# Kernel optimization log

Hardware: AMD Instinct MI355X
Metric: run time of the kernel (lower is better)

## Reference

```python
import jax, jax.numpy as jnp
import numpy as np

B, C, H = 32, 1, 384
K = 378  # cropped size per ProbaV cPSNR spec
NSHIFT = 7  # u, v each in [0, 7)


def _crops(target):
    # 49 shifted 378x378 crops of the HR target -> [49, B, C, K, K]
    return jnp.stack([target[:, :, u:u + K, v:v + K]
                      for u in range(NSHIFT) for v in range(NSHIFT)])


def setup_inputs() -> dict:
    key = jax.random.key(0)
    k1, k2, k3 = jax.random.split(key, 3)
    # scale to [0, 255) so the HR > 5 validity mask is nontrivial
    pred = jax.random.uniform(k1, (B, C, H, H), dtype=jnp.float32) * 255.0
    target = jax.random.uniform(k2, (B, C, H, H), dtype=jnp.float32) * 255.0
    blended_target = jax.random.uniform(k3, (B, C, H, H), dtype=jnp.float32) * 255.0
    return {"pred": pred, "target": target, "blended_target": blended_target}


def reference(pred, target, blended_target):
    # SR: center crop of the super-resolved prediction
    SR = pred[:, :, 3:3 + K, 3:3 + K]                      # [B, C, K, K]
    HR = _crops(target)                                     # [49, B, C, K, K]
    mask = (HR > 5.0).astype(SR.dtype)                      # validity mask per shift
    denom = jnp.sum(mask, axis=(1, 2, 3, 4))                # [49]
    co = 1.0 / denom
    # brightness bias b per shift (masked mean of HR - SR)
    b = co * jnp.sum((HR - SR) * mask, axis=(1, 2, 3, 4))   # [49]
    diff = HR - SR - b[:, None, None, None, None]
    # NOTE: torch code sums the squared error over ALL pixels (unmasked),
    # scaled by 1/num_valid -- replicated faithfully here.
    cmses = co * jnp.sum(diff * diff, axis=(1, 2, 3, 4))    # [49]
    idx = jnp.argmin(cmses)                                  # first min, like strict '<' loop
    cMSE = cmses[idx]
    cPSNR = -10.0 * jnp.log10(cMSE)
    HR_best = HR[idx]                                        # [B, C, K, K]
    # ListedLoss('l1', reduction='mean') -> mean absolute error
    MAE = jnp.mean(jnp.abs(SR - HR_best))
    return (cPSNR, MAE)
```

## Files before the change

kernel.cpp:

```cpp
#include <hip/hip_runtime.h>
#include <math.h>

#define HH 384
#define H2 (HH*HH)
#define NIMG 32
#define KK 378
#define NSH 49
#define NTOTD 4572288.0

#define SEGW 14
#define NSEG 27
#define NSLOT 9
#define GR 2
#define TR 18
#define NTILE 21
#define NBLK1 (NIMG*NTILE)
#define NACT (NSEG*NSLOT)
#define LDS_STRIDE 386

typedef float v2f __attribute__((ext_vector_type(2)));

#define OFF_PART   0
#define OFF_ROWOUT (OFF_PART + 100*NBLK1)
#define OFF_WPART  (OFF_ROWOUT + 12288*52)
#define OFF_CORRD  (OFF_WPART + 12544)
#define OFF_MISC   (OFF_CORRD + 200)

__device__ __forceinline__ float wred(float x) {
    x += __int_as_float(__builtin_amdgcn_update_dpp(0, __float_as_int(x), 0x111, 0xf, 0xf, true));
    x += __int_as_float(__builtin_amdgcn_update_dpp(0, __float_as_int(x), 0x112, 0xf, 0xf, true));
    x += __int_as_float(__builtin_amdgcn_update_dpp(0, __float_as_int(x), 0x114, 0xf, 0xf, true));
    x += __int_as_float(__builtin_amdgcn_update_dpp(0, __float_as_int(x), 0x118, 0xf, 0xf, true));
    x += __int_as_float(__builtin_amdgcn_update_dpp(0, __float_as_int(x), 0x142, 0xa, 0xf, true));
    x += __int_as_float(__builtin_amdgcn_update_dpp(0, __float_as_int(x), 0x143, 0xc, 0xf, true));
    return x;
}

__global__ __launch_bounds__(256) void k_corr(
    const float* __restrict__ pred, const float* __restrict__ targ,
    float* __restrict__ part)
{
    __shared__ v2f lds_t[(TR + 6) * LDS_STRIDE];
    __shared__ float red[100];

    const int bid = blockIdx.x;
    const int img = bid / NTILE;
    const int tile = bid - img * NTILE;
    const int r0 = tile * TR;
    const int tid = threadIdx.x;
    const int lane = tid & 63;

    if (tid < 100) red[tid] = 0.0f;

    const float* timg = targ + (size_t)img * H2;
    for (int k = 0; k < 9; ++k) {
        int i = tid + k * 256;
        int r = i / 96, c4 = (i - r * 96) * 4;
        const float4 t4 = *reinterpret_cast<const float4*>(timg + (r0 + r) * HH + c4);
        int base = r * LDS_STRIDE + c4;
        lds_t[base + 0] = (v2f){t4.x, t4.x > 5.0f ? 1.0f : 0.0f};
        lds_t[base + 1] = (v2f){t4.y, t4.y > 5.0f ? 1.0f : 0.0f};
        lds_t[base + 2] = (v2f){t4.z, t4.z > 5.0f ? 1.0f : 0.0f};
        lds_t[base + 3] = (v2f){t4.w, t4.w > 5.0f ? 1.0f : 0.0f};
    }

    const bool valid = tid < NACT;
    int seg  = valid ? tid % NSEG : NSEG - 1;
    int slot = valid ? tid / NSEG : NSLOT - 1;
    const int c0 = seg * SEGW;
    const int slot2 = slot * GR;

    float p_[GR][SEGW];
    float sp = 0.0f, sp2 = 0.0f;
    const float* pimg = pred + (size_t)img * H2;
#pragma unroll
    for (int dr = 0; dr < GR; ++dr) {
        const float* prow = pimg + (size_t)(3 + r0 + slot2 + dr) * HH + 3 + c0;
#pragma unroll
        for (int c = 0; c < SEGW; ++c) {
            float pv = prow[c];
            p_[dr][c] = pv;
            sp += pv;
            sp2 = fmaf(pv, pv, sp2);
        }
    }

    v2f acc[NSH];
#pragma unroll
    for (int i = 0; i < NSH; ++i) acc[i] = (v2f){0.0f, 0.0f};

    __syncthreads();

#pragma unroll
    for (int g = 0; g < GR + 6; ++g) {
        v2f win[SEGW + 6];
        const int wbase = (slot2 + g) * LDS_STRIDE + c0;
#pragma unroll
        for (int c = 0; c < SEGW + 6; ++c) win[c] = lds_t[wbase + c];
#pragma unroll
        for (int dr = 0; dr < GR; ++dr) {
            const int u = g - dr;
            if (u < 0 || u > 6) continue;
#pragma unroll
            for (int c = 0; c < SEGW; ++c) {
                const float pv = p_[dr][c];
                const v2f pvv = (v2f){pv, pv};
#pragma unroll
                for (int v = 0; v < 7; ++v)
                    acc[u * 7 + v] += win[v + c] * pvv;
            }
        }
        __builtin_amdgcn_sched_barrier(0);
    }

    const float vf = valid ? 1.0f : 0.0f;
    sp *= vf; sp2 *= vf;
#pragma unroll
    for (int i = 0; i < NSH; ++i) {
        float rx = wred(acc[i].x * vf);
        float ry = wred(acc[i].y * vf);
        if (lane == 63) { atomicAdd(&red[2 * i], rx); atomicAdd(&red[2 * i + 1], ry); }
    }
    {
        float rs = wred(sp), rs2 = wred(sp2);
        if (lane == 63) { atomicAdd(&red[98], rs); atomicAdd(&red[99], rs2); }
    }
    __syncthreads();
    if (tid < 100) part[(size_t)tid * NBLK1 + bid] = red[tid];
}

__global__ __launch_bounds__(256) void k_rows(
    const float* __restrict__ targ, float* __restrict__ rowout)
{
    const int tid = threadIdx.x;
    const int w = tid >> 6, lane = tid & 63;
    const int row = blockIdx.x * 4 + w;
    const int img = row / HH, y = row - img * HH;
    const float* tr = targ + (size_t)img * H2 + (size_t)y * HH;
    float* ro = rowout + (size_t)row * 52;

    float s0 = 0, s1 = 0, s2 = 0, s3 = 0;
#pragma unroll
    for (int j = 0; j < 6; ++j) {
        int x = lane + 64 * j;
        float t = tr[x];
        float m = t > 5.0f ? 1.0f : 0.0f;
        float t2 = t * t, tm = t * m;
        s0 += t; s1 += t2; s2 += tm; s3 += m;
        if (j == 0 && lane < 6) {
            ro[4 + x * 4 + 0] = t; ro[4 + x * 4 + 1] = t2;
            ro[4 + x * 4 + 2] = tm; ro[4 + x * 4 + 3] = m;
        }
        if (j == 5 && lane >= 58) {
            int k = x - 378;
            ro[28 + k * 4 + 0] = t; ro[28 + k * 4 + 1] = t2;
            ro[28 + k * 4 + 2] = tm; ro[28 + k * 4 + 3] = m;
        }
    }
    s0 = wred(s0); s1 = wred(s1); s2 = wred(s2); s3 = wred(s3);
    if (lane == 63) { ro[0] = s0; ro[1] = s1; ro[2] = s2; ro[3] = s3; }
}

__global__ __launch_bounds__(384) void k_cols(
    const float* __restrict__ rowout, double* __restrict__ wpart)
{
    __shared__ double sd[384][4];
    __shared__ float hb[6][4], tb[6][4];
    const int img = blockIdx.x / 7, v = blockIdx.x - img * 7;
    const int y = threadIdx.x;

    const float* rp = rowout + ((size_t)img * HH + y) * 52;
    float4 r4[13];
#pragma unroll
    for (int i = 0; i < 13; ++i) r4[i] = reinterpret_cast<const float4*>(rp)[i];
    const float* rf = reinterpret_cast<const float*>(r4);

    float rw[4];
#pragma unroll
    for (int q = 0; q < 4; ++q) rw[q] = rf[q];
    for (int j = 0; j < v; ++j)
#pragma unroll
        for (int q = 0; q < 4; ++q) rw[q] -= rf[4 + j * 4 + q];
    for (int k = v; k < 6; ++k)
#pragma unroll
        for (int q = 0; q < 4; ++q) rw[q] -= rf[28 + k * 4 + q];

#pragma unroll
    for (int q = 0; q < 4; ++q) sd[y][q] = (double)rw[q];
    if (y < 6)
#pragma unroll
        for (int q = 0; q < 4; ++q) hb[y][q] = rw[q];
    if (y >= KK)
#pragma unroll
        for (int q = 0; q < 4; ++q) tb[y - KK][q] = rw[q];
    __syncthreads();

    for (int s = 192; s >= 3; s >>= 1) {
        if (y < s)
#pragma unroll
            for (int q = 0; q < 4; ++q) sd[y][q] += sd[y + s][q];
        __syncthreads();
    }

    if (y < 28) {
        int u = y >> 2, q = y & 3;
        double a = sd[0][q] + sd[1][q] + sd[2][q];
        for (int j = 0; j < u; ++j) a -= (double)hb[j][q];
        for (int k = u; k < 6; ++k) a -= (double)tb[k][q];
        wpart[((size_t)(u * 7 + v) * 4 + q) * 32 + img] = a;
    }
}

__global__ __launch_bounds__(256) void k_red(
    const float* __restrict__ part, double* __restrict__ corrD)
{
    __shared__ double sd[256];
    const int q = blockIdx.x;
    const int t = threadIdx.x;
    const float* pp = part + (size_t)q * NBLK1;
    double a = (double)pp[t] + (double)pp[t + 256];
    if (t < NBLK1 - 512) a += (double)pp[t + 512];
    sd[t] = a;
    __syncthreads();
    for (int s = 128; s > 0; s >>= 1) {
        if (t < s) sd[t] += sd[t + s];
        __syncthreads();
    }
    if (t == 0) corrD[q] = sd[0];
}

__global__ __launch_bounds__(256) void k_fin(
    const double* __restrict__ corrD, const double* __restrict__ wpart,
    float* __restrict__ out, int* __restrict__ misc)
{
    __shared__ double Wd[NSH][4];
    __shared__ double cm[NSH];
    const int t = threadIdx.x;

    if (t < 196) {
        const double* wp = wpart + (size_t)t * 32;
        double a0 = 0, a1 = 0;
#pragma unroll
        for (int i = 0; i < 32; i += 2) { a0 += wp[i]; a1 += wp[i + 1]; }
        Wd[t >> 2][t & 3] = a0 + a1;
    }
    __syncthreads();
    if (t < NSH) {
        double tp = corrD[2 * t], mp = corrD[2 * t + 1];
        double Sp = corrD[98], Sp2 = corrD[99];
        double b = (Wd[t][2] - mp) / Wd[t][3];
        double s1 = Wd[t][0] - Sp;
        double s2t = Wd[t][1] - 2.0 * tp + Sp2;
        cm[t] = (s2t - 2.0 * b * s1 + NTOTD * b * b) / Wd[t][3];
    }
    __syncthreads();
    if (t == 0) {
        double best = cm[0]; int bi = 0;
        for (int s = 1; s < NSH; ++s)
            if (cm[s] < best) { best = cm[s]; bi = s; }
        out[0] = (float)(-10.0 * log10(best));
        out[1] = 0.0f;
        misc[0] = bi;
    }
}

__global__ __launch_bounds__(256) void k_mae(
    const float* __restrict__ pred, const float* __restrict__ targ,
    const int* __restrict__ misc, float* __restrict__ out)
{
    __shared__ float ps[4];
    const int idx = misc[0];
    const int u = idx / 7, v = idx - u * 7;
    const int tid = threadIdx.x;
    const int lane = tid & 63, w = tid >> 6;
    const int total = NIMG * KK * KK;
    float s = 0.0f;
    for (int i = blockIdx.x * 256 + tid; i < total; i += gridDim.x * 256) {
        int img = i / (KK * KK);
        int rem = i - img * (KK * KK);
        int r = rem / KK, c = rem - r * KK;
        float t = targ[(size_t)img * H2 + (size_t)(r + u) * HH + (c + v)];
        float p = pred[(size_t)img * H2 + (size_t)(r + 3) * HH + (c + 3)];
        s += fabsf(t - p);
    }
    s = wred(s);
    if (lane == 63) ps[w] = s;
    __syncthreads();
    if (tid == 0)
        atomicAdd(&out[1], (ps[0] + ps[1] + ps[2] + ps[3]) * (float)(1.0 / NTOTD));
}

extern "C" void kernel_launch(void* const* d_in, const int* in_sizes, int n_in,
                              void* d_out, int out_size, void* d_ws, size_t ws_size,
                              hipStream_t stream) {
    const float* pred = (const float*)d_in[0];
    const float* targ = (const float*)d_in[1];
    float* w = (float*)d_ws;
    float*  part   = w + OFF_PART;
    float*  rowout = w + OFF_ROWOUT;
    double* wpart  = (double*)(w + OFF_WPART);
    double* corrD  = (double*)(w + OFF_CORRD);
    int*    misc   = (int*)(w + OFF_MISC);
    float* out = (float*)d_out;

    k_corr<<<NBLK1, 256, 0, stream>>>(pred, targ, part);
    k_rows<<<12288 / 4, 256, 0, stream>>>(targ, rowout);
    k_cols<<<NIMG * 7, 384, 0, stream>>>(rowout, wpart);
    k_red<<<100, 256, 0, stream>>>(part, corrD);
    k_fin<<<1, 256, 0, stream>>>(corrD, wpart, out, misc);
    k_mae<<<1024, 256, 0, stream>>>(pred, targ, misc, out);
}
```

Measured before the change: 180.5 us.

## Compute MAE for all shifts speculatively and split correlation into three kernels

Drops the serial MAE kernel that had to wait for the argmin. A templated correlation kernel is launched three times: target·pred products, mask·pred products, and |target−pred| sums for all 49 shifts. The final kernel picks the MAE at the best index. Tiles shrink to 9 rows with one pred row per thread and scalar accumulators, so more blocks fit per CU. The row-sum buffer is also slimmed by storing only t and m at the edges. The cost is roughly three times the correlation work and three passes over the target and pred data, in exchange for removing the dependent gather pass.

```diff
diff --git a/kernel.cpp b/kernel.cpp
--- a/kernel.cpp
+++ b/kernel.cpp
@@ -11,20 +11,17 @@
 #define SEGW 14
 #define NSEG 27
 #define NSLOT 9
-#define GR 2
-#define TR 18
-#define NTILE 21
-#define NBLK1 (NIMG*NTILE)
+#define TRR 9
+#define NTIL 42
+#define NB2 (NIMG*NTIL)
 #define NACT (NSEG*NSLOT)
-#define LDS_STRIDE 386
-
-typedef float v2f __attribute__((ext_vector_type(2)));
+#define SROWS (TRR+6)
+#define LSF 388
 
 #define OFF_PART   0
-#define OFF_ROWOUT (OFF_PART + 100*NBLK1)
-#define OFF_WPART  (OFF_ROWOUT + 12288*52)
+#define OFF_ROWOUT (OFF_PART + 149*NB2)
+#define OFF_WPART  (OFF_ROWOUT + 12288*28)
 #define OFF_CORRD  (OFF_WPART + 12544)
-#define OFF_MISC   (OFF_CORRD + 200)
 
 __device__ __forceinline__ float wred(float x) {
     x += __int_as_float(__builtin_amdgcn_update_dpp(0, __float_as_int(x), 0x111, 0xf, 0xf, true));
@@ -36,97 +33,94 @@
     return x;
 }
 
-__global__ __launch_bounds__(256) void k_corr(
+template<int MODE>
+__global__ __launch_bounds__(256, 4) void k_corrq(
     const float* __restrict__ pred, const float* __restrict__ targ,
     float* __restrict__ part)
 {
-    __shared__ v2f lds_t[(TR + 6) * LDS_STRIDE];
-    __shared__ float red[100];
+    __shared__ float lds[SROWS * LSF];
+    __shared__ float red[51][4];
 
     const int bid = blockIdx.x;
-    const int img = bid / NTILE;
-    const int tile = bid - img * NTILE;
-    const int r0 = tile * TR;
+    const int img = bid / NTIL;
+    const int tile = bid - img * NTIL;
+    const int r0 = tile * TRR;
     const int tid = threadIdx.x;
     const int lane = tid & 63;
-
-    if (tid < 100) red[tid] = 0.0f;
+    const int wave = tid >> 6;
 
     const float* timg = targ + (size_t)img * H2;
-    for (int k = 0; k < 9; ++k) {
-        int i = tid + k * 256;
+    for (int i = tid; i < SROWS * 96; i += 256) {
         int r = i / 96, c4 = (i - r * 96) * 4;
-        const float4 t4 = *reinterpret_cast<const float4*>(timg + (r0 + r) * HH + c4);
-        int base = r * LDS_STRIDE + c4;
-        lds_t[base + 0] = (v2f){t4.x, t4.x > 5.0f ? 1.0f : 0.0f};
-        lds_t[base + 1] = (v2f){t4.y, t4.y > 5.0f ? 1.0f : 0.0f};
-        lds_t[base + 2] = (v2f){t4.z, t4.z > 5.0f ? 1.0f : 0.0f};
-        lds_t[base + 3] = (v2f){t4.w, t4.w > 5.0f ? 1.0f : 0.0f};
+        float4 t4 = *reinterpret_cast<const float4*>(timg + (r0 + r) * HH + c4);
+        if (MODE == 1) {
+            t4.x = t4.x > 5.0f ? 1.0f : 0.0f;
+            t4.y = t4.y > 5.0f ? 1.0f : 0.0f;
+            t4.z = t4.z > 5.0f ? 1.0f : 0.0f;
+            t4.w = t4.w > 5.0f ? 1.0f : 0.0f;
+        }
+        *reinterpret_cast<float4*>(&lds[r * LSF + c4]) = t4;
     }
 
     const bool valid = tid < NACT;
-    int seg  = valid ? tid % NSEG : NSEG - 1;
-    int slot = valid ? tid / NSEG : NSLOT - 1;
+    const int seg  = valid ? tid % NSEG : NSEG - 1;
+    const int slot = valid ? tid / NSEG : NSLOT - 1;
     const int c0 = seg * SEGW;
-    const int slot2 = slot * GR;
-
-    float p_[GR][SEGW];
+
+    float p_[SEGW];
     float sp = 0.0f, sp2 = 0.0f;
-    const float* pimg = pred + (size_t)img * H2;
-#pragma unroll
-    for (int dr = 0; dr < GR; ++dr) {
-        const float* prow = pimg + (size_t)(3 + r0 + slot2 + dr) * HH + 3 + c0;
+    {
+        const float* prow = pred + (size_t)img * H2 + (size_t)(3 + r0 + slot) * HH + 3 + c0;
 #pragma unroll
         for (int c = 0; c < SEGW; ++c) {
             float pv = prow[c];
-            p_[dr][c] = pv;
-            sp += pv;
-            sp2 = fmaf(pv, pv, sp2);
-        }
-    }
-
-    v2f acc[NSH];
-#pragma unroll
-    for (int i = 0; i < NSH; ++i) acc[i] = (v2f){0.0f, 0.0f};
-
-    __syncthreads();
-
-#pragma unroll
-    for (int g = 0; g < GR + 6; ++g) {
-        v2f win[SEGW + 6];
-        const int wbase = (slot2 + g) * LDS_STRIDE + c0;
-#pragma unroll
-        for (int c = 0; c < SEGW + 6; ++c) win[c] = lds_t[wbase + c];
-#pragma unroll
-        for (int dr = 0; dr < GR; ++dr) {
-            const int u = g - dr;
-            if (u < 0 || u > 6) continue;
-#pragma unroll
-            for (int c = 0; c < SEGW; ++c) {
-                const float pv = p_[dr][c];
-                const v2f pvv = (v2f){pv, pv};
-#pragma unroll
-                for (int v = 0; v < 7; ++v)
-                    acc[u * 7 + v] += win[v + c] * pvv;
+            p_[c] = pv;
+            if (MODE == 0) { sp += pv; sp2 = fmaf(pv, pv, sp2); }
+        }
+    }
+
+    float acc[NSH];
+#pragma unroll
+    for (int i = 0; i < NSH; ++i) acc[i] = 0.0f;
+
+    __syncthreads();
+
+#pragma unroll
+    for (int u = 0; u < 7; ++u) {
+        float win[SEGW + 6];
+        const int wb = (slot + u) * LSF + c0;
+#pragma unroll
+        for (int c = 0; c < SEGW + 6; ++c) win[c] = lds[wb + c];
+#pragma unroll
+        for (int c = 0; c < SEGW; ++c) {
+            const float pv = p_[c];
+#pragma unroll
+            for (int v = 0; v < 7; ++v) {
+                if (MODE == 2) acc[u * 7 + v] += fabsf(win[v + c] - pv);
+                else           acc[u * 7 + v] = fmaf(win[v + c], pv, acc[u * 7 + v]);
             }
         }
-        __builtin_amdgcn_sched_barrier(0);
     }
 
     const float vf = valid ? 1.0f : 0.0f;
-    sp *= vf; sp2 *= vf;
 #pragma unroll
     for (int i = 0; i < NSH; ++i) {
-        float rx = wred(acc[i].x * vf);
-        float ry = wred(acc[i].y * vf);
-        if (lane == 63) { atomicAdd(&red[2 * i], rx); atomicAdd(&red[2 * i + 1], ry); }
-    }
-    {
-        float rs = wred(sp), rs2 = wred(sp2);
-        if (lane == 63) { atomicAdd(&red[98], rs); atomicAdd(&red[99], rs2); }
-    }
-    __syncthreads();
-    if (tid < 100) part[(size_t)tid * NBLK1 + bid] = red[tid];
+        float r = wred(acc[i] * vf);
+        if (lane == 63) red[i][wave] = r;
+    }
+    if (MODE == 0) {
+        float rs = wred(sp * vf), rs2 = wred(sp2 * vf);
+        if (lane == 63) { red[49][wave] = rs; red[50][wave] = rs2; }
+    }
+    __syncthreads();
+
+    const int nred = (MODE == 0) ? 51 : 49;
+    if (tid < nred) {
+        int row = (MODE == 0) ? (tid < 49 ? tid : 147 + (tid - 49))
+                              : (MODE == 1 ? 49 + tid : 98 + tid);
+        part[(size_t)row * NB2 + bid] =
+            red[tid][0] + red[tid][1] + red[tid][2] + red[tid][3];
+    }
 }
 
 __global__ __launch_bounds__(256) void k_rows(
@@ -137,7 +131,7 @@
     const int row = blockIdx.x * 4 + w;
     const int img = row / HH, y = row - img * HH;
     const float* tr = targ + (size_t)img * H2 + (size_t)y * HH;
-    float* ro = rowout + (size_t)row * 52;
+    float* ro = rowout + (size_t)row * 28;
 
     float s0 = 0, s1 = 0, s2 = 0, s3 = 0;
 #pragma unroll
@@ -145,16 +139,11 @@
         int x = lane + 64 * j;
         float t = tr[x];
         float m = t > 5.0f ? 1.0f : 0.0f;
-        float t2 = t * t, tm = t * m;
-        s0 += t; s1 += t2; s2 += tm; s3 += m;
-        if (j == 0 && lane < 6) {
-            ro[4 + x * 4 + 0] = t; ro[4 + x * 4 + 1] = t2;
-            ro[4 + x * 4 + 2] = tm; ro[4 + x * 4 + 3] = m;
-        }
+        s0 += t; s1 = fmaf(t, t, s1); s2 = fmaf(t, m, s2); s3 += m;
+        if (j == 0 && lane < 6) { ro[4 + x * 2] = t; ro[5 + x * 2] = m; }
         if (j == 5 && lane >= 58) {
             int k = x - 378;
-            ro[28 + k * 4 + 0] = t; ro[28 + k * 4 + 1] = t2;
-            ro[28 + k * 4 + 2] = tm; ro[28 + k * 4 + 3] = m;
+            ro[16 + k * 2] = t; ro[17 + k * 2] = m;
         }
     }
     s0 = wred(s0); s1 = wred(s1); s2 = wred(s2); s3 = wred(s3);
@@ -169,21 +158,23 @@
     const int img = blockIdx.x / 7, v = blockIdx.x - img * 7;
     const int y = threadIdx.x;
 
-    const float* rp = rowout + ((size_t)img * HH + y) * 52;
-    float4 r4[13];
-#pragma unroll
-    for (int i = 0; i < 13; ++i) r4[i] = reinterpret_cast<const float4*>(rp)[i];
+    const float* rp = rowout + ((size_t)img * HH + y) * 28;
+    float4 r4[7];
+#pragma unroll
+    for (int i = 0; i < 7; ++i) r4[i] = reinterpret_cast<const float4*>(rp)[i];
     const float* rf = reinterpret_cast<const float*>(r4);
 
     float rw[4];
 #pragma unroll
     for (int q = 0; q < 4; ++q) rw[q] = rf[q];
-    for (int j = 0; j < v; ++j)
-#pragma unroll
-        for (int q = 0; q < 4; ++q) rw[q] -= rf[4 + j * 4 + q];
-    for (int k = v; k < 6; ++k)
-#pragma unroll
-        for (int q = 0; q < 4; ++q) rw[q] -= rf[28 + k * 4 + q];
+    for (int j = 0; j < v; ++j) {
+        float t = rf[4 + j * 2], m = rf[5 + j * 2];
+        rw[0] -= t; rw[1] -= t * t; rw[2] -= t * m; rw[3] -= m;
+    }
+    for (int k = v; k < 6; ++k) {
+        float t = rf[16 + k * 2], m = rf[17 + k * 2];
+        rw[0] -= t; rw[1] -= t * t; rw[2] -= t * m; rw[3] -= m;
+    }
 
 #pragma unroll
     for (int q = 0; q < 4; ++q) sd[y][q] = (double)rw[q];
@@ -217,9 +208,10 @@
     __shared__ double sd[256];
     const int q = blockIdx.x;
     const int t = threadIdx.x;
-    const float* pp = part + (size_t)q * NBLK1;
-    double a = (double)pp[t] + (double)pp[t + 256];
-    if (t < NBLK1 - 512) a += (double)pp[t + 512];
+    const float* pp = part + (size_t)q * NB2;
+    double a = (double)pp[t] + (double)pp[t + 256] + (double)pp[t + 512]
+             + (double)pp[t + 768] + (double)pp[t + 1024];
+    if (t < NB2 - 1280) a += (double)pp[t + 1280];
     sd[t] = a;
     __syncthreads();
     for (int s = 128; s > 0; s >>= 1) {
@@ -231,7 +223,7 @@
 
 __global__ __launch_bounds__(256) void k_fin(
     const double* __restrict__ corrD, const double* __restrict__ wpart,
-    float* __restrict__ out, int* __restrict__ misc)
+    float* __restrict__ out)
 {
     __shared__ double Wd[NSH][4];
     __shared__ double cm[NSH];
@@ -246,8 +238,8 @@
     }
     __syncthreads();
     if (t < NSH) {
-        double tp = corrD[2 * t], mp = corrD[2 * t + 1];
-        double Sp = corrD[98], Sp2 = corrD[99];
+        double tp = corrD[t], mp = corrD[49 + t];
+        double Sp = corrD[147], Sp2 = corrD[148];
         double b = (Wd[t][2] - mp) / Wd[t][3];
         double s1 = Wd[t][0] - Sp;
         double s2t = Wd[t][1] - 2.0 * tp + Sp2;
@@ -259,35 +251,8 @@
         for (int s = 1; s < NSH; ++s)
             if (cm[s] < best) { best = cm[s]; bi = s; }
         out[0] = (float)(-10.0 * log10(best));
-        out[1] = 0.0f;
-        misc[0] = bi;
-    }
-}
-
-__global__ __launch_bounds__(256) void k_mae(
-    const float* __restrict__ pred, const float* __restrict__ targ,
-    const int* __restrict__ misc, float* __restrict__ out)
-{
-    __shared__ float ps[4];
-    const int idx = misc[0];
-    const int u = idx / 7, v = idx - u * 7;
-    const int tid = threadIdx.x;
-    const int lane = tid & 63, w = tid >> 6;
-    const int total = NIMG * KK * KK;
-    float s = 0.0f;
-    for (int i = blockIdx.x * 256 + tid; i < total; i += gridDim.x * 256) {
-        int img = i / (KK * KK);
-        int rem = i - img * (KK * KK);
-        int r = rem / KK, c = rem - r * KK;
-        float t = targ[(size_t)img * H2 + (size_t)(r + u) * HH + (c + v)];
-        float p = pred[(size_t)img * H2 + (size_t)(r + 3) * HH + (c + 3)];
-        s += fabsf(t - p);
-    }
-    s = wred(s);
-    if (lane == 63) ps[w] = s;
-    __syncthreads();
-    if (tid == 0)
-        atomicAdd(&out[1], (ps[0] + ps[1] + ps[2] + ps[3]) * (float)(1.0 / NTOTD));
+        out[1] = (float)(corrD[98 + bi] / NTOTD);
+    }
 }
 
 extern "C" void kernel_launch(void* const* d_in, const int* in_sizes, int n_in,
@@ -300,13 +265,13 @@
     float*  rowout = w + OFF_ROWOUT;
     double* wpart  = (double*)(w + OFF_WPART);
     double* corrD  = (double*)(w + OFF_CORRD);
-    int*    misc   = (int*)(w + OFF_MISC);
     float* out = (float*)d_out;
 
-    k_corr<<<NBLK1, 256, 0, stream>>>(pred, targ, part);
+    k_corrq<0><<<NB2, 256, 0, stream>>>(pred, targ, part);
+    k_corrq<1><<<NB2, 256, 0, stream>>>(pred, targ, part);
+    k_corrq<2><<<NB2, 256, 0, stream>>>(pred, targ, part);
     k_rows<<<12288 / 4, 256, 0, stream>>>(targ, rowout);
     k_cols<<<NIMG * 7, 384, 0, stream>>>(rowout, wpart);
-    k_red<<<100, 256, 0, stream>>>(part, corrD);
-    k_fin<<<1, 256, 0, stream>>>(corrD, wpart, out, misc);
-    k_mae<<<1024, 256, 0, stream>>>(pred, targ, misc, out);
-}
+    k_red<<<149, 256, 0, stream>>>(part, corrD);
+    k_fin<<<1, 256, 0, stream>>>(corrD, wpart, out);
+}
```

Result: slower. 234.9 us (+30.1%).
